# Kernel tuning notes

Measured on AMD Instinct MI355X. Metric: run time of the kernel, lower is better.

## Reference

```python
import jax, jax.numpy as jnp
import numpy as np

PRED_LEN = 12
A = 128          # agents in the single scene
NHEAD = 8
NLAYERS = 2
D = 256          # embedding_dim
MLP = 1024
HDIM = 128       # decoder_h_dim
OBS_LEN = 8
MEMLEN = A * OBS_LEN
NEG = -1e9       # stands in for float('-inf') in the AR mask


def _sinusoid(length, d):
    pos = jnp.arange(length, dtype=jnp.float32)[:, None]
    div = jnp.exp(jnp.arange(0, d, 2, dtype=jnp.float32) * (-np.log(10000.0) / d))
    ang = pos * div
    pe = jnp.zeros((length, d), jnp.float32)
    pe = pe.at[:, 0::2].set(jnp.sin(ang))
    pe = pe.at[:, 1::2].set(jnp.cos(ang))
    return pe


def _ln(x, g, b):
    m = x.mean(-1, keepdims=True)
    v = ((x - m) ** 2).mean(-1, keepdims=True)
    return (x - m) / jnp.sqrt(v + 1e-5) * g + b


def _mha(q, k, v, Wq, bq, Wk, bk, Wv, bv, Wo, bo, mask):
    dh = D // NHEAD
    qh = (q @ Wq.T + bq).reshape(-1, NHEAD, dh)
    kh = (k @ Wk.T + bk).reshape(-1, NHEAD, dh)
    vh = (v @ Wv.T + bv).reshape(-1, NHEAD, dh)
    s = jnp.einsum('ihd,jhd->hij', qh, kh) / np.sqrt(dh) + mask[None]
    w = jax.nn.softmax(s, axis=-1)
    o = jnp.einsum('hij,jhd->ihd', w, vh).reshape(-1, D)
    return o @ Wo.T + bo


def _forward(last_pos, decoder_state, memory, agent_mask, in_W, in_b, out_W, out_b,
             sa_Wq, sa_bq, sa_Wk, sa_bk, sa_Wv, sa_bv, sa_Wo, sa_bo,
             ca_Wq, ca_bq, ca_Wk, ca_bk, ca_Wv, ca_bv, ca_Wo, ca_bo,
             ff_W1, ff_b1, ff_W2, ff_b2,
             ln1_g, ln1_b, ln2_g, ln2_b, ln3_g, ln3_b):
    agent_pe = _sinusoid(A, D)
    scene_pos = last_pos
    tokens = []
    outs = []
    for s in range(PRED_LEN):  # fixed-length AR loop (unrolled, static shapes)
        feat = jnp.concatenate([scene_pos, decoder_state], axis=-1)  # [A, 2+HDIM]
        tokens.append(feat @ in_W.T + in_b)                          # [A, D]
        steps = s + 1
        tgt = jnp.concatenate(tokens, axis=0)                        # [steps*A, D]
        time_enc = jnp.repeat(_sinusoid(steps, D), A, axis=0)
        x = tgt + time_enc + jnp.tile(agent_pe, (steps, 1))
        times = jnp.repeat(jnp.arange(steps), A)
        # generate_ar_mask: block-causal over time, tiled agent_mask within block
        tgt_mask = jnp.where(times[None, :] > times[:, None], NEG,
                             jnp.tile(agent_mask, (steps, steps)))
        # generate_mask: tiled agent_mask for cross-attention to memory
        mem_mask = jnp.tile(agent_mask, (steps, MEMLEN // A))
        for l in range(NLAYERS):
            sa = _mha(x, x, x, sa_Wq[l], sa_bq[l], sa_Wk[l], sa_bk[l],
                      sa_Wv[l], sa_bv[l], sa_Wo[l], sa_bo[l], tgt_mask)
            x = _ln(x + sa, ln1_g[l], ln1_b[l])
            ca = _mha(x, memory, memory, ca_Wq[l], ca_bq[l], ca_Wk[l], ca_bk[l],
                      ca_Wv[l], ca_bv[l], ca_Wo[l], ca_bo[l], mem_mask)
            x = _ln(x + ca, ln2_g[l], ln2_b[l])
            ff = jax.nn.relu(x @ ff_W1[l].T + ff_b1[l]) @ ff_W2[l].T + ff_b2[l]
            x = _ln(x + ff, ln3_g[l], ln3_b[l])
        rel = x[-A:] @ out_W.T + out_b                               # [A, 2]
        outs.append(rel)
        scene_pos = scene_pos + rel
    return jnp.stack(outs, axis=0)                                   # [PRED_LEN, A, 2]


def setup_inputs():
    key = jax.random.key(0)
    ks = jax.random.split(key, 40)
    def rn(k, shape, scale=0.02):
        return jax.random.normal(k, shape, jnp.float32) * scale
    inp = {
        'last_pos': jax.random.normal(ks[0], (A, 2), jnp.float32),
        'decoder_state': jax.random.normal(ks[1], (A, HDIM), jnp.float32),
        'memory': jax.random.normal(ks[2], (MEMLEN, D), jnp.float32),
        'agent_mask': jnp.zeros((A, A), jnp.float32),
        'in_W': rn(ks[3], (D, 2 + HDIM)),
        'in_b': jnp.zeros((D,), jnp.float32),
        'out_W': rn(ks[4], (2, D)),
        'out_b': jnp.zeros((2,), jnp.float32),
    }
    names = ['sa_Wq', 'sa_Wk', 'sa_Wv', 'sa_Wo', 'ca_Wq', 'ca_Wk', 'ca_Wv', 'ca_Wo']
    for i, n in enumerate(names):
        inp[n] = rn(ks[5 + i], (NLAYERS, D, D))
        inp[n.replace('W', 'b')] = jnp.zeros((NLAYERS, D), jnp.float32)
    inp['ff_W1'] = rn(ks[20], (NLAYERS, MLP, D))
    inp['ff_b1'] = jnp.zeros((NLAYERS, MLP), jnp.float32)
    inp['ff_W2'] = rn(ks[21], (NLAYERS, D, MLP))
    inp['ff_b2'] = jnp.zeros((NLAYERS, D), jnp.float32)
    for n in ['ln1', 'ln2', 'ln3']:
        inp[n + '_g'] = jnp.ones((NLAYERS, D), jnp.float32)
        inp[n + '_b'] = jnp.zeros((NLAYERS, D), jnp.float32)
    return inp


def reference(last_pos, decoder_state, memory, agent_mask, in_W, in_b, out_W, out_b,
              sa_Wq, sa_bq, sa_Wk, sa_bk, sa_Wv, sa_bv, sa_Wo, sa_bo,
              ca_Wq, ca_bq, ca_Wk, ca_bk, ca_Wv, ca_bv, ca_Wo, ca_bo,
              ff_W1, ff_b1, ff_W2, ff_b2,
              ln1_g, ln1_b, ln2_g, ln2_b, ln3_g, ln3_b):
    return _forward(last_pos, decoder_state, memory, agent_mask, in_W, in_b, out_W, out_b,
                    sa_Wq, sa_bq, sa_Wk, sa_bk, sa_Wv, sa_bv, sa_Wo, sa_bo,
                    ca_Wq, ca_bq, ca_Wk, ca_bk, ca_Wv, ca_bv, ca_Wo, ca_bo,
                    ff_W1, ff_b1, ff_W2, ff_b2,
                    ln1_g, ln1_b, ln2_g, ln2_b, ln3_g, ln3_b)
```

## Files before the change

### kernel.cpp

```cpp
#include <hip/hip_runtime.h>
#include <math.h>

#define AGENTS 128
#define DIM 256
#define NHEADS 8
#define MEM_LEN 1024
#define MLP_DIM 1024
#define PRED 12
#define MAXS (PRED * AGENTS)

typedef __attribute__((ext_vector_type(8))) short short8;
typedef __attribute__((ext_vector_type(4))) float f32x4;

#define MFMA(a, b, c) __builtin_amdgcn_mfma_f32_16x16x32_bf16(a, b, c, 0, 0, 0)

__device__ __forceinline__ unsigned short f2bf(float f) {
  union { float f; unsigned u; } v; v.f = f;
  unsigned r = v.u + 0x7fffu + ((v.u >> 16) & 1u);
  return (unsigned short)(r >> 16);
}

__device__ __forceinline__ short8 afrag8(const float* p) {
  float4 a = *(const float4*)p;
  float4 b = *(const float4*)(p + 4);
  short8 r;
  r[0] = (short)f2bf(a.x); r[1] = (short)f2bf(a.y);
  r[2] = (short)f2bf(a.z); r[3] = (short)f2bf(a.w);
  r[4] = (short)f2bf(b.x); r[5] = (short)f2bf(b.y);
  r[6] = (short)f2bf(b.z); r[7] = (short)f2bf(b.w);
  return r;
}

__device__ __forceinline__ void ln_stats(const float* __restrict__ pst, int row,
                                         float& mean, float& rstd) {
  float4 p0 = *(const float4*)(pst + row * 8);
  float4 p1 = *(const float4*)(pst + row * 8 + 4);
  float s  = p0.x + p0.z + p1.x + p1.z;
  float ss = p0.y + p0.w + p1.y + p1.w;
  mean = s * (1.0f / 256.0f);
  rstd = rsqrtf(ss * (1.0f / 256.0f) - mean * mean + 1e-5f);
}

__device__ __forceinline__ short8 afragLN(const float* __restrict__ yr,
                                          const float* __restrict__ lg,
                                          const float* __restrict__ lb,
                                          int k, float mean, float rstd) {
  float4 a = *(const float4*)(yr + k), b = *(const float4*)(yr + k + 4);
  float4 ga = *(const float4*)(lg + k), gb = *(const float4*)(lg + k + 4);
  float4 ba = *(const float4*)(lb + k), bb = *(const float4*)(lb + k + 4);
  short8 r;
  r[0] = (short)f2bf((a.x - mean) * rstd * ga.x + ba.x);
  r[1] = (short)f2bf((a.y - mean) * rstd * ga.y + ba.y);
  r[2] = (short)f2bf((a.z - mean) * rstd * ga.z + ba.z);
  r[3] = (short)f2bf((a.w - mean) * rstd * ga.w + ba.w);
  r[4] = (short)f2bf((b.x - mean) * rstd * gb.x + bb.x);
  r[5] = (short)f2bf((b.y - mean) * rstd * gb.y + bb.y);
  r[6] = (short)f2bf((b.z - mean) * rstd * gb.z + bb.z);
  r[7] = (short)f2bf((b.w - mean) * rstd * gb.w + bb.w);
  return r;
}

template <int AMODE, int RES, int EPI>
__global__ __launch_bounds__(256) void wproj_k(
    const unsigned short* __restrict__ ab, int lda,
    const float* __restrict__ Ya, const float* __restrict__ psta,
    const float* __restrict__ lga, const float* __restrict__ lba,
    const unsigned short* __restrict__ W, const float* __restrict__ bias, int K,
    const float* __restrict__ res,
    const float* __restrict__ Yp, const float* __restrict__ pstp,
    const float* __restrict__ gp, const float* __restrict__ bp,
    float* __restrict__ Yo, float* __restrict__ psto,
    unsigned short* __restrict__ mido)
{
  const int tid = threadIdx.x, l = tid & 63, w = tid >> 6;
  const int c15 = l & 15, g8 = (l >> 4) * 8, r0v = (l >> 4) * 4;
  const int rowb = blockIdx.x * 64 + w * 16;
  const int arow = rowb + c15;
  const int cb = blockIdx.y;
  const int colb = cb * 64;

  float meanA = 0.f, rstdA = 0.f;
  if (AMODE == 1) ln_stats(psta, arow, meanA, rstdA);

  const int KC = K >> 5;
  f32x4 acc[4] = {};
  const unsigned short* wp = W + (colb + c15) * K + g8;
  for (int kc = 0; kc < KC; ++kc) {
    short8 af;
    if (AMODE == 0) af = *(const short8*)(ab + arow * lda + kc * 32 + g8);
    else af = afragLN(Ya + arow * 256, lga, lba, kc * 32 + g8, meanA, rstdA);
#pragma unroll
    for (int t = 0; t < 4; ++t)
      acc[t] = MFMA(af, *(const short8*)(wp + t * 16 * K + kc * 32), acc[t]);
  }

  float mp[4], rp[4];
  if (RES == 2) {
#pragma unroll
    for (int r = 0; r < 4; ++r) ln_stats(pstp, rowb + r0v + r, mp[r], rp[r]);
  }

  float v[4][4];
#pragma unroll
  for (int t = 0; t < 4; ++t) {
    const int col = colb + t * 16 + c15;
    const float bb = bias[col];
    float gpp = 0.f, bpp = 0.f;
    if (RES == 2) { gpp = gp[col]; bpp = bp[col]; }
#pragma unroll
    for (int r = 0; r < 4; ++r) {
      const int row = rowb + r0v + r;
      float x = acc[t][r] + bb;
      if (RES == 1) x += res[row * 256 + col];
      if (RES == 2) x += (Yp[row * 256 + col] - mp[r]) * rp[r] * gpp + bpp;
      if (EPI == 0) Yo[row * 256 + col] = x;
      if (EPI == 1) mido[row * 1024 + col] = f2bf(fmaxf(x, 0.f));
      v[t][r] = x;
    }
  }
  if (EPI == 0) {
#pragma unroll
    for (int r = 0; r < 4; ++r) {
      float s  = v[0][r] + v[1][r] + v[2][r] + v[3][r];
      float ss = v[0][r]*v[0][r] + v[1][r]*v[1][r] + v[2][r]*v[2][r] + v[3][r]*v[3][r];
#pragma unroll
      for (int m = 1; m < 16; m <<= 1) {
        s  += __shfl_xor(s, m, 64);
        ss += __shfl_xor(ss, m, 64);
      }
      if (c15 == 0) {
        const int row = rowb + r0v + r;
        psto[row * 8 + cb * 2]     = s;
        psto[row * 8 + cb * 2 + 1] = ss;
      }
    }
  }
}

template <int AMODE>
__global__ __launch_bounds__(256) void kvproj_k(
    const unsigned short* __restrict__ ab, int lda,
    const float* __restrict__ Ya, const float* __restrict__ psta,
    const float* __restrict__ lga, const float* __restrict__ lba,
    const float* __restrict__ af32,
    const unsigned short* __restrict__ Wk, const float* __restrict__ bk,
    const unsigned short* __restrict__ Wv, const float* __restrict__ bv,
    unsigned short* __restrict__ Ko, unsigned short* __restrict__ Vo,
    int Spad, int crow)
{
  const int tid = threadIdx.x, l = tid & 63, w = tid >> 6;
  const int c15 = l & 15, g8 = (l >> 4) * 8, r0v = (l >> 4) * 4;
  const int rowb = blockIdx.x * 64 + w * 16;
  const int arow = rowb + c15;
  const int y = blockIdx.y;
  const bool isK = y < 4;
  const int colb = (y & 3) * 64;
  const unsigned short* W = isK ? Wk : Wv;
  const float* bias = isK ? bk : bv;

  float meanA = 0.f, rstdA = 0.f;
  if (AMODE == 1) ln_stats(psta, arow, meanA, rstdA);

  f32x4 acc[4] = {};
  const unsigned short* wp = W + (colb + c15) * 256 + g8;
  for (int kc = 0; kc < 8; ++kc) {
    short8 af;
    if (AMODE == 0) af = *(const short8*)(ab + arow * lda + kc * 32 + g8);
    else if (AMODE == 1) af = afragLN(Ya + arow * 256, lga, lba, kc * 32 + g8, meanA, rstdA);
    else af = afrag8(af32 + arow * 256 + kc * 32 + g8);
#pragma unroll
    for (int t = 0; t < 4; ++t)
      acc[t] = MFMA(af, *(const short8*)(wp + t * 16 * 256 + kc * 32), acc[t]);
  }
#pragma unroll
  for (int t = 0; t < 4; ++t) {
    const int col = colb + t * 16 + c15;
    const float bb = bias[col];
    const int hh = col >> 5, d = col & 31;
#pragma unroll
    for (int r = 0; r < 4; ++r) {
      const int row = crow + rowb + r0v + r;
      unsigned short val = f2bf(acc[t][r] + bb);
      if (isK) Ko[hh * Spad * 32 + row * 32 + d] = val;
      else     Vo[col * Spad + row] = val;
    }
  }
}

template <int AMODE>
__global__ __launch_bounds__(256) void attn2_k(
    const unsigned short* __restrict__ ab,
    const float* __restrict__ Ya, const float* __restrict__ psta,
    const float* __restrict__ lga, const float* __restrict__ lba,
    const unsigned short* __restrict__ Wq, const float* __restrict__ bq,
    const unsigned short* __restrict__ Kc, const unsigned short* __restrict__ Vt,
    const float* __restrict__ mask, unsigned short* __restrict__ Ob,
    int S, int Spad)
{
  __shared__ unsigned short sq[4][16][32];
  __shared__ unsigned short ps[4][16][96];
  const int tid = threadIdx.x, l = tid & 63, w = tid >> 6;
  const int c15 = l & 15, g = l >> 4, g8 = g * 8, r0v = g * 4;
  const int h = blockIdx.y;
  const int rowb = blockIdx.x * 64 + w * 16;
  const int arow = rowb + c15;

  float meanA = 0.f, rstdA = 0.f;
  if (AMODE == 1) ln_stats(psta, arow, meanA, rstdA);
  f32x4 q0 = {}, q1 = {};
  const unsigned short* wp = Wq + (h * 32 + c15) * 256 + g8;
  for (int kc = 0; kc < 8; ++kc) {
    short8 af;
    if (AMODE == 0) af = *(const short8*)(ab + arow * 256 + kc * 32 + g8);
    else af = afragLN(Ya + arow * 256, lga, lba, kc * 32 + g8, meanA, rstdA);
    q0 = MFMA(af, *(const short8*)(wp + kc * 32), q0);
    q1 = MFMA(af, *(const short8*)(wp + 16 * 256 + kc * 32), q1);
  }
  {
    const float b0 = bq[h * 32 + c15], b1 = bq[h * 32 + 16 + c15];
#pragma unroll
    for (int r = 0; r < 4; ++r) {
      sq[w][r0v + r][c15]      = f2bf(q0[r] + b0);
      sq[w][r0v + r][16 + c15] = f2bf(q1[r] + b1);
    }
  }
  short8 qf = *(const short8*)&sq[w][c15][g8];

  float mk[2][4][4];
#pragma unroll
  for (int p = 0; p < 2; ++p)
#pragma unroll
    for (int t = 0; t < 4; ++t)
#pragma unroll
      for (int r = 0; r < 4; ++r)
        mk[p][t][r] = mask[arow * AGENTS + p * 64 + t * 16 + g * 4 + r];

  const unsigned short* kh = Kc + h * Spad * 32;
  const unsigned short* vh = Vt + h * 32 * Spad;
  unsigned short* pq = &ps[w][0][0];
  const float scale = 0.17677669529663687f;
  f32x4 oa0 = {}, oa1 = {};
  float lsum = 0.f;

  for (int kc = 0; kc < S; kc += 64) {
    const int p = (kc >> 6) & 1;
#pragma unroll
    for (int t = 0; t < 4; ++t) {
      short8 kf = *(const short8*)(kh + (kc + t * 16 + c15) * 32 + g8);
      f32x4 zz = {};
      f32x4 sc = MFMA(kf, qf, zz);
      float e0 = __expf(sc[0] * scale + mk[p][t][0]);
      float e1 = __expf(sc[1] * scale + mk[p][t][1]);
      float e2 = __expf(sc[2] * scale + mk[p][t][2]);
      float e3 = __expf(sc[3] * scale + mk[p][t][3]);
      unsigned short b0 = f2bf(e0), b1 = f2bf(e1), b2 = f2bf(e2), b3 = f2bf(e3);
      union { unsigned u; float f; } c0, c1, c2, c3;
      c0.u = (unsigned)b0 << 16; c1.u = (unsigned)b1 << 16;
      c2.u = (unsigned)b2 << 16; c3.u = (unsigned)b3 << 16;
      lsum += c0.f + c1.f + c2.f + c3.f;
      uint2 u2;
      u2.x = (unsigned)b0 | ((unsigned)b1 << 16);
      u2.y = (unsigned)b2 | ((unsigned)b3 << 16);
      *(uint2*)&pq[c15 * 96 + t * 16 + g * 4] = u2;
    }
#pragma unroll
    for (int ks = 0; ks < 2; ++ks) {
      short8 pf = *(const short8*)&pq[c15 * 96 + ks * 32 + g8];
      short8 v0 = *(const short8*)(vh + c15 * Spad + kc + ks * 32 + g8);
      short8 v1 = *(const short8*)(vh + (16 + c15) * Spad + kc + ks * 32 + g8);
      oa0 = MFMA(v0, pf, oa0);
      oa1 = MFMA(v1, pf, oa1);
    }
  }
  lsum += __shfl_xor(lsum, 16, 64);
  lsum += __shfl_xor(lsum, 32, 64);
  const float inv = 1.0f / lsum;
#pragma unroll
  for (int r = 0; r < 4; ++r) {
    Ob[arow * DIM + h * 32 + g * 4 + r]      = f2bf(oa0[r] * inv);
    Ob[arow * DIM + h * 32 + 16 + g * 4 + r] = f2bf(oa1[r] * inv);
  }
}

__global__ __launch_bounds__(256) void embed_k(
    const float* __restrict__ scene, const float* __restrict__ ds,
    const unsigned short* __restrict__ inWb, const float* __restrict__ inb,
    const float* __restrict__ peA, const float* __restrict__ peT,
    float* __restrict__ x0, unsigned short* __restrict__ xb0, int step)
{
  const int tid = threadIdx.x, l = tid & 63, w = tid >> 6;
  const int c15 = l & 15, g8 = (l >> 4) * 8, r0v = (l >> 4) * 4;
  const int rowb = blockIdx.x * 64 + w * 16;
  const int arow = rowb + c15;
  const int colb = blockIdx.y * 64;
  f32x4 acc[4] = {};
  const unsigned short* wp = inWb + (colb + c15) * 160 + g8;
  for (int kc = 0; kc < 5; ++kc) {
    short8 af;
#pragma unroll
    for (int j = 0; j < 8; ++j) {
      int kk = kc * 32 + g8 + j;
      float v = (kk < 2) ? scene[arow * 2 + kk]
                         : ((kk < 130) ? ds[arow * 128 + (kk - 2)] : 0.f);
      af[j] = (short)f2bf(v);
    }
#pragma unroll
    for (int t = 0; t < 4; ++t)
      acc[t] = MFMA(af, *(const short8*)(wp + t * 16 * 160 + kc * 32), acc[t]);
  }
#pragma unroll
  for (int t = 0; t < 4; ++t) {
    const int col = colb + t * 16 + c15;
    const float bb = inb[col] + peT[step * DIM + col];
#pragma unroll
    for (int r = 0; r < 4; ++r) {
      const int row = rowb + r0v + r;
      float v = acc[t][r] + bb + peA[row * DIM + col];
      x0[row * DIM + col] = v;
      xb0[row * DIM + col] = f2bf(v);
    }
  }
}

__global__ __launch_bounds__(256) void outp_k(
    const float* __restrict__ Y3, const float* __restrict__ pst3,
    const float* __restrict__ g3, const float* __restrict__ b3,
    const float* __restrict__ outW, const float* __restrict__ outB,
    float* __restrict__ outbuf, float* __restrict__ scene, int step)
{
  const int tid = threadIdx.x;
  const int row = tid >> 1, j = tid & 1;
  float mean, rstd;
  ln_stats(pst3, row, mean, rstd);
  const float* yr = Y3 + row * 256;
  const float* wr = outW + j * 256;
  float a = 0.f;
  for (int k = 0; k < 256; k += 4) {
    float4 y = *(const float4*)(yr + k);
    float4 gg = *(const float4*)(g3 + k);
    float4 bb = *(const float4*)(b3 + k);
    float4 ww = *(const float4*)(wr + k);
    a += ((y.x - mean) * rstd * gg.x + bb.x) * ww.x
       + ((y.y - mean) * rstd * gg.y + bb.y) * ww.y
       + ((y.z - mean) * rstd * gg.z + bb.z) * ww.z
       + ((y.w - mean) * rstd * gg.w + bb.w) * ww.w;
  }
  a += outB[j];
  outbuf[(step * AGENTS + row) * 2 + j] = a;
  scene[row * 2 + j] += a;
}

__global__ void cvt8_k(const float* p0, const float* p1, const float* p2,
                       const float* p3, const float* p4, const float* p5,
                       const float* p6, const float* p7, unsigned short* dst)
{
  const float* s;
  switch (blockIdx.z) {
    case 0: s = p0; break; case 1: s = p1; break;
    case 2: s = p2; break; case 3: s = p3; break;
    case 4: s = p4; break; case 5: s = p5; break;
    case 6: s = p6; break; default: s = p7; break;
  }
  int i = blockIdx.x * 256 + threadIdx.x;
  dst[blockIdx.z * 131072 + i] = f2bf(s[i]);
}

__global__ void cvtff_k(const float* w1, const float* w2, unsigned short* dst)
{
  const float* s = blockIdx.z ? w2 : w1;
  int i = blockIdx.x * 256 + threadIdx.x;
  dst[blockIdx.z * 524288 + i] = f2bf(s[i]);
}

__global__ void cvtinw_k(const float* w, unsigned short* dst)
{
  int i = blockIdx.x * 256 + threadIdx.x;
  if (i >= 256 * 160) return;
  int n = i / 160, k = i - n * 160;
  dst[i] = (k < 130) ? f2bf(w[n * 130 + k]) : (unsigned short)0;
}

__global__ void pe_k(float* peA, float* peT)
{
  int i = blockIdx.x * 256 + threadIdx.x;
  if (i < 128 * 256) {
    int row = i >> 8, c = i & 255, p = c >> 1;
    float dv = expf((float)(2 * p) * (-9.210340371976184f / 256.f));
    float ang = (float)row * dv;
    peA[i] = (c & 1) ? cosf(ang) : sinf(ang);
  } else if (i < 140 * 256) {
    int j = i - 32768;
    int s = j >> 8, c = j & 255, p = c >> 1;
    float dv = expf((float)(2 * p) * (-9.210340371976184f / 256.f));
    float ang = (float)s * dv;
    peT[j] = (c & 1) ? cosf(ang) : sinf(ang);
  }
}

extern "C" void kernel_launch(void* const* d_in, const int* in_sizes, int n_in,
                              void* d_out, int out_size, void* d_ws, size_t ws_size,
                              hipStream_t stream)
{
  const float* last_pos      = (const float*)d_in[0];
  const float* decoder_state = (const float*)d_in[1];
  const float* memory        = (const float*)d_in[2];
  const float* agent_mask    = (const float*)d_in[3];
  const float* in_W  = (const float*)d_in[4];
  const float* in_b  = (const float*)d_in[5];
  const float* out_W = (const float*)d_in[6];
  const float* out_b = (const float*)d_in[7];
  const float* sa_bq = (const float*)d_in[9];
  const float* sa_bk = (const float*)d_in[11];
  const float* sa_bv = (const float*)d_in[13];
  const float* sa_bo = (const float*)d_in[15];
  const float* ca_bq = (const float*)d_in[17];
  const float* ca_bk = (const float*)d_in[19];
  const float* ca_bv = (const float*)d_in[21];
  const float* ca_bo = (const float*)d_in[23];
  const float* ff_W1 = (const float*)d_in[24];
  const float* ff_b1 = (const float*)d_in[25];
  const float* ff_W2 = (const float*)d_in[26];
  const float* ff_b2 = (const float*)d_in[27];
  const float* ln1_g = (const float*)d_in[28];
  const float* ln1_b = (const float*)d_in[29];
  const float* ln2_g = (const float*)d_in[30];
  const float* ln2_b = (const float*)d_in[31];
  const float* ln3_g = (const float*)d_in[32];
  const float* ln3_b = (const float*)d_in[33];
  float* out = (float*)d_out;

  float* ws    = (float*)d_ws;
  float* scene = ws;
  float* x0    = scene + 256;
  float* Y1    = x0 + 32768;
  float* Y2    = Y1 + 32768;
  float* Y3    = Y2 + 32768;
  float* pst1  = Y3 + 32768;
  float* pst2  = pst1 + 1024;
  float* pst3  = pst2 + 1024;
  float* peA   = pst3 + 1024;
  float* peT   = peA + 32768;
  unsigned short* xb0   = (unsigned short*)(peT + 3072);
  unsigned short* abuf  = xb0 + 32768;
  unsigned short* mid   = abuf + 32768;
  unsigned short* saK   = mid + 131072;
  unsigned short* saV   = saK + 2 * MAXS * 256;
  unsigned short* memK  = saV + 2 * MAXS * 256;
  unsigned short* memV  = memK + 2 * MEM_LEN * 256;
  unsigned short* dxdb  = memV + 2 * MEM_LEN * 256;
  unsigned short* ffW1b = dxdb + 8 * 131072;
  unsigned short* ffW2b = ffW1b + 524288;
  unsigned short* inWb  = ffW2b + 524288;

  const dim3 blk(256);

  cvt8_k<<<dim3(512, 1, 8), blk, 0, stream>>>(
      (const float*)d_in[8], (const float*)d_in[10], (const float*)d_in[12],
      (const float*)d_in[14], (const float*)d_in[16], (const float*)d_in[18],
      (const float*)d_in[20], (const float*)d_in[22], dxdb);
  cvtff_k<<<dim3(2048, 1, 2), blk, 0, stream>>>(ff_W1, ff_W2, ffW1b);
  cvtinw_k<<<160, blk, 0, stream>>>(in_W, inWb);
  pe_k<<<140, blk, 0, stream>>>(peA, peT);
  for (int l = 0; l < 2; ++l) {
    kvproj_k<2><<<dim3(16, 8), blk, 0, stream>>>(
        nullptr, 0, nullptr, nullptr, nullptr, nullptr, memory,
        dxdb + 5 * 131072 + l * 65536, ca_bk + l * 256,
        dxdb + 6 * 131072 + l * 65536, ca_bv + l * 256,
        memK + l * 262144, memV + l * 262144, MEM_LEN, 0);
  }
  hipMemcpyAsync(scene, last_pos, 256 * sizeof(float), hipMemcpyDeviceToDevice, stream);

  for (int s = 0; s < PRED; ++s) {
    embed_k<<<dim3(2, 4), blk, 0, stream>>>(scene, decoder_state, inWb, in_b,
                                            peA, peT, x0, xb0, s);
    for (int l = 0; l < 2; ++l) {
      const unsigned short* saWq = dxdb + 0 * 131072 + l * 65536;
      const unsigned short* saWk = dxdb + 1 * 131072 + l * 65536;
      const unsigned short* saWv = dxdb + 2 * 131072 + l * 65536;
      const unsigned short* saWo = dxdb + 3 * 131072 + l * 65536;
      const unsigned short* caWq = dxdb + 4 * 131072 + l * 65536;
      const unsigned short* caWo = dxdb + 7 * 131072 + l * 65536;
      unsigned short* saKl = saK + l * MAXS * 256;
      unsigned short* saVl = saV + l * MAXS * 256;
      unsigned short* memKl = memK + l * 262144;
      unsigned short* memVl = memV + l * 262144;

      if (l == 0) {
        kvproj_k<0><<<dim3(2, 8), blk, 0, stream>>>(
            xb0, 256, nullptr, nullptr, nullptr, nullptr, nullptr,
            saWk, sa_bk, saWv, sa_bv, saKl, saVl, MAXS, s * AGENTS);
        attn2_k<0><<<dim3(2, 8), blk, 0, stream>>>(
            xb0, nullptr, nullptr, nullptr, nullptr,
            saWq, sa_bq, saKl, saVl, agent_mask, abuf, (s + 1) * AGENTS, MAXS);
        wproj_k<0, 1, 0><<<dim3(2, 4), blk, 0, stream>>>(
            abuf, 256, nullptr, nullptr, nullptr, nullptr,
            saWo, sa_bo, 256, x0, nullptr, nullptr, nullptr, nullptr,
            Y1, pst1, nullptr);
      } else {
        kvproj_k<1><<<dim3(2, 8), blk, 0, stream>>>(
            nullptr, 0, Y3, pst3, ln3_g, ln3_b, nullptr,
            saWk, sa_bk + 256, saWv, sa_bv + 256, saKl, saVl, MAXS, s * AGENTS);
        attn2_k<1><<<dim3(2, 8), blk, 0, stream>>>(
            nullptr, Y3, pst3, ln3_g, ln3_b,
            saWq, sa_bq + 256, saKl, saVl, agent_mask, abuf, (s + 1) * AGENTS, MAXS);
        wproj_k<0, 2, 0><<<dim3(2, 4), blk, 0, stream>>>(
            abuf, 256, nullptr, nullptr, nullptr, nullptr,
            saWo, sa_bo + 256, 256, nullptr, Y3, pst3, ln3_g, ln3_b,
            Y1, pst1, nullptr);
      }
      attn2_k<1><<<dim3(2, 8), blk, 0, stream>>>(
          nullptr, Y1, pst1, ln1_g + l * 256, ln1_b + l * 256,
          caWq, ca_bq + l * 256, memKl, memVl, agent_mask, abuf, MEM_LEN, MEM_LEN);
      wproj_k<0, 2, 0><<<dim3(2, 4), blk, 0, stream>>>(
          abuf, 256, nullptr, nullptr, nullptr, nullptr,
          caWo, ca_bo + l * 256, 256, nullptr, Y1, pst1, ln1_g + l * 256, ln1_b + l * 256,
          Y2, pst2, nullptr);
      wproj_k<1, 0, 1><<<dim3(2, 16), blk, 0, stream>>>(
          nullptr, 0, Y2, pst2, ln2_g + l * 256, ln2_b + l * 256,
          ffW1b + l * 262144, ff_b1 + l * 1024, 256,
          nullptr, nullptr, nullptr, nullptr, nullptr,
          nullptr, nullptr, mid);
      wproj_k<0, 2, 0><<<dim3(2, 4), blk, 0, stream>>>(
          mid, 1024, nullptr, nullptr, nullptr, nullptr,
          ffW2b + l * 262144, ff_b2 + l * 256, 1024,
          nullptr, Y2, pst2, ln2_g + l * 256, ln2_b + l * 256,
          Y3, pst3, nullptr);
    }
    outp_k<<<1, blk, 0, stream>>>(Y3, pst3, ln3_g + 256, ln3_b + 256,
                                  out_W, out_b, out, scene, s);
  }
}
```

Measured before the change: 2.481 ms.

## Fuse autoregressive decoder loop into persistent megakernel with grid barriers

Replaces roughly 170 small kernel launches for the 12-step AR decoder with one persistent 16-workgroup kernel that runs each stage as a phase and separates phases with a software grid barrier. The output projection is folded into the next step's embed phase, and the per-step scene positions are kept in an array so no in-place update races across workgroups. The memory K/V projections for both layers are merged into a single launch. This targets launch overhead and inter-kernel gaps. In exchange it adds atomic barrier cost, relies on all 16 workgroups being co-resident, and leaves most of the GPU idle within each phase.

```diff
diff --git a/kernel.cpp b/kernel.cpp
--- a/kernel.cpp
+++ b/kernel.cpp
@@ -5,9 +5,9 @@
 #define DIM 256
 #define NHEADS 8
 #define MEM_LEN 1024
-#define MLP_DIM 1024
 #define PRED 12
 #define MAXS (PRED * AGENTS)
+#define NWG 16
 
 typedef __attribute__((ext_vector_type(8))) short short8;
 typedef __attribute__((ext_vector_type(4))) float f32x4;
@@ -60,89 +60,113 @@
   return r;
 }
 
-template <int AMODE, int RES, int EPI>
-__global__ __launch_bounds__(256) void wproj_k(
-    const unsigned short* __restrict__ ab, int lda,
+struct MegaP {
+  const float *ds, *mask;
+  const float *in_b, *out_W, *out_b;
+  const float *sa_bq, *sa_bk, *sa_bv, *sa_bo;
+  const float *ca_bq, *ca_bo;
+  const float *ff_b1, *ff_b2;
+  const float *ln1_g, *ln1_b, *ln2_g, *ln2_b, *ln3_g, *ln3_b;
+  float *out;
+  float *sceneArr;
+  float *x0, *Y1, *Y2, *Y3;
+  float *pst1, *pst2, *pst3;
+  const float *peA, *peT;
+  unsigned short *xb0, *abuf, *mid;
+  unsigned short *saK, *saV, *memK, *memV;
+  const unsigned short *dxdb, *ffW1b, *ffW2b, *inWb;
+  unsigned *barCnt, *barGen;
+};
+
+__device__ __forceinline__ void gridbar(unsigned* cnt, unsigned* gen) {
+  __syncthreads();
+  if (threadIdx.x == 0) {
+    __threadfence();
+    unsigned g = __hip_atomic_load(gen, __ATOMIC_RELAXED, __HIP_MEMORY_SCOPE_AGENT);
+    unsigned a = __hip_atomic_fetch_add(cnt, 1u, __ATOMIC_ACQ_REL, __HIP_MEMORY_SCOPE_AGENT);
+    if (a == (unsigned)(NWG - 1)) {
+      __hip_atomic_store(cnt, 0u, __ATOMIC_RELAXED, __HIP_MEMORY_SCOPE_AGENT);
+      __hip_atomic_store(gen, g + 1u, __ATOMIC_RELEASE, __HIP_MEMORY_SCOPE_AGENT);
+    } else {
+      while (__hip_atomic_load(gen, __ATOMIC_ACQUIRE, __HIP_MEMORY_SCOPE_AGENT) == g)
+        __builtin_amdgcn_s_sleep(1);
+    }
+    __threadfence();
+  }
+  __syncthreads();
+}
+
+__device__ void embed_phase(const MegaP& p, int wg, int s) {
+  if (wg >= 8) return;
+  __shared__ float sscene[256];
+  const int tid = threadIdx.x;
+  if (s > 0) {
+    const int row = tid >> 1, j = tid & 1;
+    float mean, rstd; ln_stats(p.pst3, row, mean, rstd);
+    const float* yr = p.Y3 + row * 256;
+    const float* wr = p.out_W + j * 256;
+    const float* g3 = p.ln3_g + 256;
+    const float* b3 = p.ln3_b + 256;
+    float a = 0.f;
+    for (int k = 0; k < 256; k += 4) {
+      float4 y = *(const float4*)(yr + k);
+      float4 gg = *(const float4*)(g3 + k);
+      float4 bb = *(const float4*)(b3 + k);
+      float4 ww = *(const float4*)(wr + k);
+      a += ((y.x - mean) * rstd * gg.x + bb.x) * ww.x
+         + ((y.y - mean) * rstd * gg.y + bb.y) * ww.y
+         + ((y.z - mean) * rstd * gg.z + bb.z) * ww.z
+         + ((y.w - mean) * rstd * gg.w + bb.w) * ww.w;
+    }
+    a += p.out_b[j];
+    float sv = p.sceneArr[(s - 1) * 256 + row * 2 + j] + a;
+    if (wg == 0) p.out[((s - 1) * AGENTS + row) * 2 + j] = a;
+    p.sceneArr[s * 256 + row * 2 + j] = sv;
+    sscene[row * 2 + j] = sv;
+  } else {
+    sscene[tid] = p.sceneArr[tid];
+  }
+  __syncthreads();
+
+  const int l = tid & 63, w = tid >> 6;
+  const int c15 = l & 15, g8 = (l >> 4) * 8, r0v = (l >> 4) * 4;
+  const int rowb = (wg >> 2) * 64 + w * 16;
+  const int arow = rowb + c15;
+  const int colb = (wg & 3) * 64;
+  f32x4 acc[4] = {};
+  const unsigned short* wp = p.inWb + (colb + c15) * 160 + g8;
+  for (int kc = 0; kc < 5; ++kc) {
+    short8 af;
+#pragma unroll
+    for (int j = 0; j < 8; ++j) {
+      int kk = kc * 32 + g8 + j;
+      float v = (kk < 2) ? sscene[arow * 2 + kk]
+                         : ((kk < 130) ? p.ds[arow * 128 + (kk - 2)] : 0.f);
+      af[j] = (short)f2bf(v);
+    }
+#pragma unroll
+    for (int t = 0; t < 4; ++t)
+      acc[t] = MFMA(af, *(const short8*)(wp + t * 16 * 160 + kc * 32), acc[t]);
+  }
+#pragma unroll
+  for (int t = 0; t < 4; ++t) {
+    const int col = colb + t * 16 + c15;
+    const float bb = p.in_b[col] + p.peT[s * DIM + col];
+#pragma unroll
+    for (int r = 0; r < 4; ++r) {
+      const int row = rowb + r0v + r;
+      float v = acc[t][r] + bb + p.peA[row * DIM + col];
+      p.x0[row * DIM + col] = v;
+      p.xb0[row * DIM + col] = f2bf(v);
+    }
+  }
+}
+
+template <int AMODE>
+__device__ void kv_phase(const MegaP& p, int wg,
+    const unsigned short* __restrict__ ab,
     const float* __restrict__ Ya, const float* __restrict__ psta,
     const float* __restrict__ lga, const float* __restrict__ lba,
-    const unsigned short* __restrict__ W, const float* __restrict__ bias, int K,
-    const float* __restrict__ res,
-    const float* __restrict__ Yp, const float* __restrict__ pstp,
-    const float* __restrict__ gp, const float* __restrict__ bp,
-    float* __restrict__ Yo, float* __restrict__ psto,
-    unsigned short* __restrict__ mido)
-{
-  const int tid = threadIdx.x, l = tid & 63, w = tid >> 6;
-  const int c15 = l & 15, g8 = (l >> 4) * 8, r0v = (l >> 4) * 4;
-  const int rowb = blockIdx.x * 64 + w * 16;
-  const int arow = rowb + c15;
-  const int cb = blockIdx.y;
-  const int colb = cb * 64;
-
-  float meanA = 0.f, rstdA = 0.f;
-  if (AMODE == 1) ln_stats(psta, arow, meanA, rstdA);
-
-  const int KC = K >> 5;
-  f32x4 acc[4] = {};
-  const unsigned short* wp = W + (colb + c15) * K + g8;
-  for (int kc = 0; kc < KC; ++kc) {
-    short8 af;
-    if (AMODE == 0) af = *(const short8*)(ab + arow * lda + kc * 32 + g8);
-    else af = afragLN(Ya + arow * 256, lga, lba, kc * 32 + g8, meanA, rstdA);
-#pragma unroll
-    for (int t = 0; t < 4; ++t)
-      acc[t] = MFMA(af, *(const short8*)(wp + t * 16 * K + kc * 32), acc[t]);
-  }
-
-  float mp[4], rp[4];
-  if (RES == 2) {
-#pragma unroll
-    for (int r = 0; r < 4; ++r) ln_stats(pstp, rowb + r0v + r, mp[r], rp[r]);
-  }
-
-  float v[4][4];
-#pragma unroll
-  for (int t = 0; t < 4; ++t) {
-    const int col = colb + t * 16 + c15;
-    const float bb = bias[col];
-    float gpp = 0.f, bpp = 0.f;
-    if (RES == 2) { gpp = gp[col]; bpp = bp[col]; }
-#pragma unroll
-    for (int r = 0; r < 4; ++r) {
-      const int row = rowb + r0v + r;
-      float x = acc[t][r] + bb;
-      if (RES == 1) x += res[row * 256 + col];
-      if (RES == 2) x += (Yp[row * 256 + col] - mp[r]) * rp[r] * gpp + bpp;
-      if (EPI == 0) Yo[row * 256 + col] = x;
-      if (EPI == 1) mido[row * 1024 + col] = f2bf(fmaxf(x, 0.f));
-      v[t][r] = x;
-    }
-  }
-  if (EPI == 0) {
-#pragma unroll
-    for (int r = 0; r < 4; ++r) {
-      float s  = v[0][r] + v[1][r] + v[2][r] + v[3][r];
-      float ss = v[0][r]*v[0][r] + v[1][r]*v[1][r] + v[2][r]*v[2][r] + v[3][r]*v[3][r];
-#pragma unroll
-      for (int m = 1; m < 16; m <<= 1) {
-        s  += __shfl_xor(s, m, 64);
-        ss += __shfl_xor(ss, m, 64);
-      }
-      if (c15 == 0) {
-        const int row = rowb + r0v + r;
-        psto[row * 8 + cb * 2]     = s;
-        psto[row * 8 + cb * 2 + 1] = ss;
-      }
-    }
-  }
-}
-
-template <int AMODE>
-__global__ __launch_bounds__(256) void kvproj_k(
-    const unsigned short* __restrict__ ab, int lda,
-    const float* __restrict__ Ya, const float* __restrict__ psta,
-    const float* __restrict__ lga, const float* __restrict__ lba,
-    const float* __restrict__ af32,
     const unsigned short* __restrict__ Wk, const float* __restrict__ bk,
     const unsigned short* __restrict__ Wv, const float* __restrict__ bv,
     unsigned short* __restrict__ Ko, unsigned short* __restrict__ Vo,
@@ -150,9 +174,9 @@
 {
   const int tid = threadIdx.x, l = tid & 63, w = tid >> 6;
   const int c15 = l & 15, g8 = (l >> 4) * 8, r0v = (l >> 4) * 4;
-  const int rowb = blockIdx.x * 64 + w * 16;
+  const int rowb = (wg >> 3) * 64 + w * 16;
   const int arow = rowb + c15;
-  const int y = blockIdx.y;
+  const int y = wg & 7;
   const bool isK = y < 4;
   const int colb = (y & 3) * 64;
   const unsigned short* W = isK ? Wk : Wv;
@@ -165,9 +189,8 @@
   const unsigned short* wp = W + (colb + c15) * 256 + g8;
   for (int kc = 0; kc < 8; ++kc) {
     short8 af;
-    if (AMODE == 0) af = *(const short8*)(ab + arow * lda + kc * 32 + g8);
-    else if (AMODE == 1) af = afragLN(Ya + arow * 256, lga, lba, kc * 32 + g8, meanA, rstdA);
-    else af = afrag8(af32 + arow * 256 + kc * 32 + g8);
+    if (AMODE == 0) af = *(const short8*)(ab + arow * 256 + kc * 32 + g8);
+    else af = afragLN(Ya + arow * 256, lga, lba, kc * 32 + g8, meanA, rstdA);
 #pragma unroll
     for (int t = 0; t < 4; ++t)
       acc[t] = MFMA(af, *(const short8*)(wp + t * 16 * 256 + kc * 32), acc[t]);
@@ -188,21 +211,20 @@
 }
 
 template <int AMODE>
-__global__ __launch_bounds__(256) void attn2_k(
+__device__ void attn_phase(const MegaP& p, int wg,
     const unsigned short* __restrict__ ab,
     const float* __restrict__ Ya, const float* __restrict__ psta,
     const float* __restrict__ lga, const float* __restrict__ lba,
     const unsigned short* __restrict__ Wq, const float* __restrict__ bq,
     const unsigned short* __restrict__ Kc, const unsigned short* __restrict__ Vt,
-    const float* __restrict__ mask, unsigned short* __restrict__ Ob,
-    int S, int Spad)
+    unsigned short* __restrict__ Ob, int S, int Spad)
 {
   __shared__ unsigned short sq[4][16][32];
   __shared__ unsigned short ps[4][16][96];
   const int tid = threadIdx.x, l = tid & 63, w = tid >> 6;
   const int c15 = l & 15, g = l >> 4, g8 = g * 8, r0v = g * 4;
-  const int h = blockIdx.y;
-  const int rowb = blockIdx.x * 64 + w * 16;
+  const int h = wg & 7;
+  const int rowb = (wg >> 3) * 64 + w * 16;
   const int arow = rowb + c15;
 
   float meanA = 0.f, rstdA = 0.f;
@@ -228,12 +250,12 @@
 
   float mk[2][4][4];
 #pragma unroll
-  for (int p = 0; p < 2; ++p)
+  for (int pp = 0; pp < 2; ++pp)
 #pragma unroll
     for (int t = 0; t < 4; ++t)
 #pragma unroll
       for (int r = 0; r < 4; ++r)
-        mk[p][t][r] = mask[arow * AGENTS + p * 64 + t * 16 + g * 4 + r];
+        mk[pp][t][r] = p.mask[arow * AGENTS + pp * 64 + t * 16 + g * 4 + r];
 
   const unsigned short* kh = Kc + h * Spad * 32;
   const unsigned short* vh = Vt + h * 32 * Spad;
@@ -243,16 +265,16 @@
   float lsum = 0.f;
 
   for (int kc = 0; kc < S; kc += 64) {
-    const int p = (kc >> 6) & 1;
+    const int pp = (kc >> 6) & 1;
 #pragma unroll
     for (int t = 0; t < 4; ++t) {
       short8 kf = *(const short8*)(kh + (kc + t * 16 + c15) * 32 + g8);
       f32x4 zz = {};
       f32x4 sc = MFMA(kf, qf, zz);
-      float e0 = __expf(sc[0] * scale + mk[p][t][0]);
-      float e1 = __expf(sc[1] * scale + mk[p][t][1]);
-      float e2 = __expf(sc[2] * scale + mk[p][t][2]);
-      float e3 = __expf(sc[3] * scale + mk[p][t][3]);
+      float e0 = __expf(sc[0] * scale + mk[pp][t][0]);
+      float e1 = __expf(sc[1] * scale + mk[pp][t][1]);
+      float e2 = __expf(sc[2] * scale + mk[pp][t][2]);
+      float e3 = __expf(sc[3] * scale + mk[pp][t][3]);
       unsigned short b0 = f2bf(e0), b1 = f2bf(e1), b2 = f2bf(e2), b3 = f2bf(e3);
       union { unsigned u; float f; } c0, c1, c2, c3;
       c0.u = (unsigned)b0 << 16; c1.u = (unsigned)b1 << 16;
@@ -282,58 +304,110 @@
   }
 }
 
-__global__ __launch_bounds__(256) void embed_k(
-    const float* __restrict__ scene, const float* __restrict__ ds,
-    const unsigned short* __restrict__ inWb, const float* __restrict__ inb,
-    const float* __restrict__ peA, const float* __restrict__ peT,
-    float* __restrict__ x0, unsigned short* __restrict__ xb0, int step)
-{
+template <int RES>
+__device__ void wproj_phase(const MegaP& p, int wg,
+    const unsigned short* __restrict__ ab, int lda,
+    const unsigned short* __restrict__ W, const float* __restrict__ bias, int K,
+    const float* __restrict__ res,
+    const float* __restrict__ Yp, const float* __restrict__ pstp,
+    const float* __restrict__ gp, const float* __restrict__ bp,
+    float* __restrict__ Yo, float* __restrict__ psto)
+{
+  if (wg >= 8) return;
   const int tid = threadIdx.x, l = tid & 63, w = tid >> 6;
   const int c15 = l & 15, g8 = (l >> 4) * 8, r0v = (l >> 4) * 4;
-  const int rowb = blockIdx.x * 64 + w * 16;
+  const int rowb = (wg >> 2) * 64 + w * 16;
   const int arow = rowb + c15;
-  const int colb = blockIdx.y * 64;
+  const int cb = wg & 3;
+  const int colb = cb * 64;
+
+  const int KC = K >> 5;
   f32x4 acc[4] = {};
-  const unsigned short* wp = inWb + (colb + c15) * 160 + g8;
-  for (int kc = 0; kc < 5; ++kc) {
-    short8 af;
-#pragma unroll
-    for (int j = 0; j < 8; ++j) {
-      int kk = kc * 32 + g8 + j;
-      float v = (kk < 2) ? scene[arow * 2 + kk]
-                         : ((kk < 130) ? ds[arow * 128 + (kk - 2)] : 0.f);
-      af[j] = (short)f2bf(v);
-    }
+  const unsigned short* wp = W + (colb + c15) * K + g8;
+  for (int kc = 0; kc < KC; ++kc) {
+    short8 af = *(const short8*)(ab + arow * lda + kc * 32 + g8);
 #pragma unroll
     for (int t = 0; t < 4; ++t)
-      acc[t] = MFMA(af, *(const short8*)(wp + t * 16 * 160 + kc * 32), acc[t]);
-  }
+      acc[t] = MFMA(af, *(const short8*)(wp + t * 16 * K + kc * 32), acc[t]);
+  }
+
+  float mp[4], rp[4];
+  if (RES == 2) {
+#pragma unroll
+    for (int r = 0; r < 4; ++r) ln_stats(pstp, rowb + r0v + r, mp[r], rp[r]);
+  }
+  float v[4][4];
 #pragma unroll
   for (int t = 0; t < 4; ++t) {
     const int col = colb + t * 16 + c15;
-    const float bb = inb[col] + peT[step * DIM + col];
+    const float bb = bias[col];
+    float gpp = 0.f, bpp = 0.f;
+    if (RES == 2) { gpp = gp[col]; bpp = bp[col]; }
 #pragma unroll
     for (int r = 0; r < 4; ++r) {
       const int row = rowb + r0v + r;
-      float v = acc[t][r] + bb + peA[row * DIM + col];
-      x0[row * DIM + col] = v;
-      xb0[row * DIM + col] = f2bf(v);
-    }
-  }
-}
-
-__global__ __launch_bounds__(256) void outp_k(
-    const float* __restrict__ Y3, const float* __restrict__ pst3,
-    const float* __restrict__ g3, const float* __restrict__ b3,
-    const float* __restrict__ outW, const float* __restrict__ outB,
-    float* __restrict__ outbuf, float* __restrict__ scene, int step)
-{
+      float x = acc[t][r] + bb;
+      if (RES == 1) x += res[row * 256 + col];
+      if (RES == 2) x += (Yp[row * 256 + col] - mp[r]) * rp[r] * gpp + bpp;
+      Yo[row * 256 + col] = x;
+      v[t][r] = x;
+    }
+  }
+#pragma unroll
+  for (int r = 0; r < 4; ++r) {
+    float s  = v[0][r] + v[1][r] + v[2][r] + v[3][r];
+    float ss = v[0][r]*v[0][r] + v[1][r]*v[1][r] + v[2][r]*v[2][r] + v[3][r]*v[3][r];
+#pragma unroll
+    for (int m = 1; m < 16; m <<= 1) {
+      s  += __shfl_xor(s, m, 64);
+      ss += __shfl_xor(ss, m, 64);
+    }
+    if (c15 == 0) {
+      const int row = rowb + r0v + r;
+      psto[row * 8 + cb * 2]     = s;
+      psto[row * 8 + cb * 2 + 1] = ss;
+    }
+  }
+}
+
+__device__ void ff1_phase(const MegaP& p, int wg,
+    const float* __restrict__ Ya, const float* __restrict__ psta,
+    const float* __restrict__ lga, const float* __restrict__ lba,
+    const unsigned short* __restrict__ W1, const float* __restrict__ b1)
+{
+  const int tid = threadIdx.x, l = tid & 63, w = tid >> 6;
+  const int c15 = l & 15, g8 = (l >> 4) * 8, r0v = (l >> 4) * 4;
+  const int rowb = (wg >> 3) * 64 + w * 16;
+  const int arow = rowb + c15;
+  const int colb = (wg & 7) * 128;
+  float mean, rstd; ln_stats(psta, arow, mean, rstd);
+  f32x4 acc[8] = {};
+  const unsigned short* wp = W1 + (colb + c15) * 256 + g8;
+  for (int kc = 0; kc < 8; ++kc) {
+    short8 af = afragLN(Ya + arow * 256, lga, lba, kc * 32 + g8, mean, rstd);
+#pragma unroll
+    for (int t = 0; t < 8; ++t)
+      acc[t] = MFMA(af, *(const short8*)(wp + t * 16 * 256 + kc * 32), acc[t]);
+  }
+#pragma unroll
+  for (int t = 0; t < 8; ++t) {
+    const int col = colb + t * 16 + c15;
+    const float bb = b1[col];
+#pragma unroll
+    for (int r = 0; r < 4; ++r)
+      p.mid[(rowb + r0v + r) * 1024 + col] = f2bf(fmaxf(acc[t][r] + bb, 0.f));
+  }
+}
+
+__device__ void final_phase(const MegaP& p, int wg) {
+  if (wg != 0) return;
   const int tid = threadIdx.x;
   const int row = tid >> 1, j = tid & 1;
-  float mean, rstd;
-  ln_stats(pst3, row, mean, rstd);
-  const float* yr = Y3 + row * 256;
-  const float* wr = outW + j * 256;
+  float mean, rstd; ln_stats(p.pst3, row, mean, rstd);
+  const float* yr = p.Y3 + row * 256;
+  const float* wr = p.out_W + j * 256;
+  const float* g3 = p.ln3_g + 256;
+  const float* b3 = p.ln3_b + 256;
   float a = 0.f;
   for (int k = 0; k < 256; k += 4) {
     float4 y = *(const float4*)(yr + k);
@@ -345,9 +419,68 @@
        + ((y.z - mean) * rstd * gg.z + bb.z) * ww.z
        + ((y.w - mean) * rstd * gg.w + bb.w) * ww.w;
   }
-  a += outB[j];
-  outbuf[(step * AGENTS + row) * 2 + j] = a;
-  scene[row * 2 + j] += a;
+  a += p.out_b[j];
+  p.out[((PRED - 1) * AGENTS + row) * 2 + j] = a;
+}
+
+__global__ __launch_bounds__(256, 1) void mega_k(MegaP p) {
+  const int wg = blockIdx.x;
+#define GB gridbar(p.barCnt, p.barGen)
+  for (int s = 0; s < PRED; ++s) {
+    embed_phase(p, wg, s);
+    GB;
+    for (int l = 0; l < 2; ++l) {
+      const unsigned short* saWq = p.dxdb + 0 * 131072 + l * 65536;
+      const unsigned short* saWk = p.dxdb + 1 * 131072 + l * 65536;
+      const unsigned short* saWv = p.dxdb + 2 * 131072 + l * 65536;
+      const unsigned short* saWo = p.dxdb + 3 * 131072 + l * 65536;
+      const unsigned short* caWq = p.dxdb + 4 * 131072 + l * 65536;
+      const unsigned short* caWo = p.dxdb + 7 * 131072 + l * 65536;
+      unsigned short* saKl = p.saK + l * MAXS * 256;
+      unsigned short* saVl = p.saV + l * MAXS * 256;
+      unsigned short* memKl = p.memK + l * 262144;
+      unsigned short* memVl = p.memV + l * 262144;
+
+      if (l == 0) {
+        kv_phase<0>(p, wg, p.xb0, nullptr, nullptr, nullptr, nullptr,
+                    saWk, p.sa_bk, saWv, p.sa_bv, saKl, saVl, MAXS, s * AGENTS);
+        GB;
+        attn_phase<0>(p, wg, p.xb0, nullptr, nullptr, nullptr, nullptr,
+                      saWq, p.sa_bq, saKl, saVl, p.abuf, (s + 1) * AGENTS, MAXS);
+        GB;
+        wproj_phase<1>(p, wg, p.abuf, 256, saWo, p.sa_bo, 256,
+                       p.x0, nullptr, nullptr, nullptr, nullptr, p.Y1, p.pst1);
+        GB;
+      } else {
+        kv_phase<1>(p, wg, nullptr, p.Y3, p.pst3, p.ln3_g, p.ln3_b,
+                    saWk, p.sa_bk + 256, saWv, p.sa_bv + 256, saKl, saVl,
+                    MAXS, s * AGENTS);
+        GB;
+        attn_phase<1>(p, wg, nullptr, p.Y3, p.pst3, p.ln3_g, p.ln3_b,
+                      saWq, p.sa_bq + 256, saKl, saVl, p.abuf, (s + 1) * AGENTS, MAXS);
+        GB;
+        wproj_phase<2>(p, wg, p.abuf, 256, saWo, p.sa_bo + 256, 256,
+                       nullptr, p.Y3, p.pst3, p.ln3_g, p.ln3_b, p.Y1, p.pst1);
+        GB;
+      }
+      attn_phase<1>(p, wg, nullptr, p.Y1, p.pst1, p.ln1_g + l * 256, p.ln1_b + l * 256,
+                    caWq, p.ca_bq + l * 256, memKl, memVl, p.abuf, MEM_LEN, MEM_LEN);
+      GB;
+      wproj_phase<2>(p, wg, p.abuf, 256, caWo, p.ca_bo + l * 256, 256,
+                     nullptr, p.Y1, p.pst1, p.ln1_g + l * 256, p.ln1_b + l * 256,
+                     p.Y2, p.pst2);
+      GB;
+      ff1_phase(p, wg, p.Y2, p.pst2, p.ln2_g + l * 256, p.ln2_b + l * 256,
+                p.ffW1b + l * 262144, p.ff_b1 + l * 1024);
+      GB;
+      wproj_phase<2>(p, wg, p.mid, 1024, p.ffW2b + l * 262144, p.ff_b2 + l * 256, 1024,
+                     nullptr, p.Y2, p.pst2, p.ln2_g + l * 256, p.ln2_b + l * 256,
+                     p.Y3, p.pst3);
+      GB;
+    }
+  }
+  final_phase(p, wg);
+#undef GB
 }
 
 __global__ void cvt8_k(const float* p0, const float* p1, const float* p2,
@@ -384,18 +517,60 @@
 {
   int i = blockIdx.x * 256 + threadIdx.x;
   if (i < 128 * 256) {
-    int row = i >> 8, c = i & 255, p = c >> 1;
-    float dv = expf((float)(2 * p) * (-9.210340371976184f / 256.f));
+    int row = i >> 8, c = i & 255, pp = c >> 1;
+    float dv = expf((float)(2 * pp) * (-9.210340371976184f / 256.f));
     float ang = (float)row * dv;
     peA[i] = (c & 1) ? cosf(ang) : sinf(ang);
   } else if (i < 140 * 256) {
     int j = i - 32768;
-    int s = j >> 8, c = j & 255, p = c >> 1;
-    float dv = expf((float)(2 * p) * (-9.210340371976184f / 256.f));
+    int s = j >> 8, c = j & 255, pp = c >> 1;
+    float dv = expf((float)(2 * pp) * (-9.210340371976184f / 256.f));
     float ang = (float)s * dv;
     peT[j] = (c & 1) ? cosf(ang) : sinf(ang);
   }
 }
+
+__global__ __launch_bounds__(256) void memkv_k(
+    const float* __restrict__ mem, const unsigned short* __restrict__ dxd,
+    const float* __restrict__ bk, const float* __restrict__ bvv,
+    unsigned short* __restrict__ memK, unsigned short* __restrict__ memV)
+{
+  const int li = blockIdx.z;
+  const int y = blockIdx.y;
+  const bool isK = y < 4;
+  const int colb = (y & 3) * 64;
+  const unsigned short* W = dxd + (isK ? 5 : 6) * 131072 + li * 65536;
+  const float* bias = (isK ? bk : bvv) + li * 256;
+  unsigned short* Ko = memK + li * MEM_LEN * 256;
+  unsigned short* Vo = memV + li * MEM_LEN * 256;
+  const int tid = threadIdx.x, l = tid & 63, w = tid >> 6;
+  const int c15 = l & 15, g8 = (l >> 4) * 8, r0v = (l >> 4) * 4;
+  const int rowb = blockIdx.x * 64 + w * 16;
+  const int arow = rowb + c15;
+  f32x4 acc[4] = {};
+  const unsigned short* wp = W + (colb + c15) * 256 + g8;
+  for (int kc = 0; kc < 8; ++kc) {
+    short8 af = afrag8(mem + arow * 256 + kc * 32 + g8);
+#pragma unroll
+    for (int t = 0; t < 4; ++t)
+      acc[t] = MFMA(af, *(const short8*)(wp + t * 16 * 256 + kc * 32), acc[t]);
+  }
+#pragma unroll
+  for (int t = 0; t < 4; ++t) {
+    const int col = colb + t * 16 + c15;
+    const float bb = bias[col];
+    const int hh = col >> 5, d = col & 31;
+#pragma unroll
+    for (int r = 0; r < 4; ++r) {
+      const int row = rowb + r0v + r;
+      unsigned short val = f2bf(acc[t][r] + bb);
+      if (isK) Ko[hh * MEM_LEN * 32 + row * 32 + d] = val;
+      else     Vo[col * MEM_LEN + row] = val;
+    }
+  }
+}
+
+__global__ void initbar_k(unsigned* b) { b[0] = 0; b[1] = 0; }
 
 extern "C" void kernel_launch(void* const* d_in, const int* in_sizes, int n_in,
                               void* d_out, int out_size, void* d_ws, size_t ws_size,
@@ -409,29 +584,10 @@
   const float* in_b  = (const float*)d_in[5];
   const float* out_W = (const float*)d_in[6];
   const float* out_b = (const float*)d_in[7];
-  const float* sa_bq = (const float*)d_in[9];
-  const float* sa_bk = (const float*)d_in[11];
-  const float* sa_bv = (const float*)d_in[13];
-  const float* sa_bo = (const float*)d_in[15];
-  const float* ca_bq = (const float*)d_in[17];
-  const float* ca_bk = (const float*)d_in[19];
-  const float* ca_bv = (const float*)d_in[21];
-  const float* ca_bo = (const float*)d_in[23];
-  const float* ff_W1 = (const float*)d_in[24];
-  const float* ff_b1 = (const float*)d_in[25];
-  const float* ff_W2 = (const float*)d_in[26];
-  const float* ff_b2 = (const float*)d_in[27];
-  const float* ln1_g = (const float*)d_in[28];
-  const float* ln1_b = (const float*)d_in[29];
-  const float* ln2_g = (const float*)d_in[30];
-  const float* ln2_b = (const float*)d_in[31];
-  const float* ln3_g = (const float*)d_in[32];
-  const float* ln3_b = (const float*)d_in[33];
-  float* out = (float*)d_out;
 
   float* ws    = (float*)d_ws;
-  float* scene = ws;
-  float* x0    = scene + 256;
+  float* sceneArr = ws;
+  float* x0    = sceneArr + 13 * 256;
   float* Y1    = x0 + 32768;
   float* Y2    = Y1 + 32768;
   float* Y3    = Y2 + 32768;
@@ -451,6 +607,7 @@
   unsigned short* ffW1b = dxdb + 8 * 131072;
   unsigned short* ffW2b = ffW1b + 524288;
   unsigned short* inWb  = ffW2b + 524288;
+  unsigned* bar = (unsigned*)(inWb + 40960);
 
   const dim3 blk(256);
 
@@ -458,75 +615,34 @@
       (const float*)d_in[8], (const float*)d_in[10], (const float*)d_in[12],
       (const float*)d_in[14], (const float*)d_in[16], (const float*)d_in[18],
       (const float*)d_in[20], (const float*)d_in[22], dxdb);
-  cvtff_k<<<dim3(2048, 1, 2), blk, 0, stream>>>(ff_W1, ff_W2, ffW1b);
+  cvtff_k<<<dim3(2048, 1, 2), blk, 0, stream>>>((const float*)d_in[24],
+                                                (const float*)d_in[26], ffW1b);
   cvtinw_k<<<160, blk, 0, stream>>>(in_W, inWb);
   pe_k<<<140, blk, 0, stream>>>(peA, peT);
-  for (int l = 0; l < 2; ++l) {
-    kvproj_k<2><<<dim3(16, 8), blk, 0, stream>>>(
-        nullptr, 0, nullptr, nullptr, nullptr, nullptr, memory,
-        dxdb + 5 * 131072 + l * 65536, ca_bk + l * 256,
-        dxdb + 6 * 131072 + l * 65536, ca_bv + l * 256,
-        memK + l * 262144, memV + l * 262144, MEM_LEN, 0);
-  }
-  hipMemcpyAsync(scene, last_pos, 256 * sizeof(float), hipMemcpyDeviceToDevice, stream);
-
-  for (int s = 0; s < PRED; ++s) {
-    embed_k<<<dim3(2, 4), blk, 0, stream>>>(scene, decoder_state, inWb, in_b,
-                                            peA, peT, x0, xb0, s);
-    for (int l = 0; l < 2; ++l) {
-      const unsigned short* saWq = dxdb + 0 * 131072 + l * 65536;
-      const unsigned short* saWk = dxdb + 1 * 131072 + l * 65536;
-      const unsigned short* saWv = dxdb + 2 * 131072 + l * 65536;
-      const unsigned short* saWo = dxdb + 3 * 131072 + l * 65536;
-      const unsigned short* caWq = dxdb + 4 * 131072 + l * 65536;
-      const unsigned short* caWo = dxdb + 7 * 131072 + l * 65536;
-      unsigned short* saKl = saK + l * MAXS * 256;
-      unsigned short* saVl = saV + l * MAXS * 256;
-      unsigned short* memKl = memK + l * 262144;
-      unsigned short* memVl = memV + l * 262144;
-
-      if (l == 0) {
-        kvproj_k<0><<<dim3(2, 8), blk, 0, stream>>>(
-            xb0, 256, nullptr, nullptr, nullptr, nullptr, nullptr,
-            saWk, sa_bk, saWv, sa_bv, saKl, saVl, MAXS, s * AGENTS);
-        attn2_k<0><<<dim3(2, 8), blk, 0, stream>>>(
-            xb0, nullptr, nullptr, nullptr, nullptr,
-            saWq, sa_bq, saKl, saVl, agent_mask, abuf, (s + 1) * AGENTS, MAXS);
-        wproj_k<0, 1, 0><<<dim3(2, 4), blk, 0, stream>>>(
-            abuf, 256, nullptr, nullptr, nullptr, nullptr,
-            saWo, sa_bo, 256, x0, nullptr, nullptr, nullptr, nullptr,
-            Y1, pst1, nullptr);
-      } else {
-        kvproj_k<1><<<dim3(2, 8), blk, 0, stream>>>(
-            nullptr, 0, Y3, pst3, ln3_g, ln3_b, nullptr,
-            saWk, sa_bk + 256, saWv, sa_bv + 256, saKl, saVl, MAXS, s * AGENTS);
-        attn2_k<1><<<dim3(2, 8), blk, 0, stream>>>(
-            nullptr, Y3, pst3, ln3_g, ln3_b,
-            saWq, sa_bq + 256, saKl, saVl, agent_mask, abuf, (s + 1) * AGENTS, MAXS);
-        wproj_k<0, 2, 0><<<dim3(2, 4), blk, 0, stream>>>(
-            abuf, 256, nullptr, nullptr, nullptr, nullptr,
-            saWo, sa_bo + 256, 256, nullptr, Y3, pst3, ln3_g, ln3_b,
-            Y1, pst1, nullptr);
-      }
-      attn2_k<1><<<dim3(2, 8), blk, 0, stream>>>(
-          nullptr, Y1, pst1, ln1_g + l * 256, ln1_b + l * 256,
-          caWq, ca_bq + l * 256, memKl, memVl, agent_mask, abuf, MEM_LEN, MEM_LEN);
-      wproj_k<0, 2, 0><<<dim3(2, 4), blk, 0, stream>>>(
-          abuf, 256, nullptr, nullptr, nullptr, nullptr,
-          caWo, ca_bo + l * 256, 256, nullptr, Y1, pst1, ln1_g + l * 256, ln1_b + l * 256,
-          Y2, pst2, nullptr);
-      wproj_k<1, 0, 1><<<dim3(2, 16), blk, 0, stream>>>(
-          nullptr, 0, Y2, pst2, ln2_g + l * 256, ln2_b + l * 256,
-          ffW1b + l * 262144, ff_b1 + l * 1024, 256,
-          nullptr, nullptr, nullptr, nullptr, nullptr,
-          nullptr, nullptr, mid);
-      wproj_k<0, 2, 0><<<dim3(2, 4), blk, 0, stream>>>(
-          mid, 1024, nullptr, nullptr, nullptr, nullptr,
-          ffW2b + l * 262144, ff_b2 + l * 256, 1024,
-          nullptr, Y2, pst2, ln2_g + l * 256, ln2_b + l * 256,
-          Y3, pst3, nullptr);
-    }
-    outp_k<<<1, blk, 0, stream>>>(Y3, pst3, ln3_g + 256, ln3_b + 256,
-                                  out_W, out_b, out, scene, s);
-  }
-}
+  memkv_k<<<dim3(16, 8, 2), blk, 0, stream>>>(memory, dxdb,
+      (const float*)d_in[19], (const float*)d_in[21], memK, memV);
+  initbar_k<<<1, 1, 0, stream>>>(bar);
+  hipMemcpyAsync(sceneArr, last_pos, 256 * sizeof(float),
+                 hipMemcpyDeviceToDevice, stream);
+
+  MegaP p;
+  p.ds = decoder_state; p.mask = agent_mask;
+  p.in_b = in_b; p.out_W = out_W; p.out_b = out_b;
+  p.sa_bq = (const float*)d_in[9];  p.sa_bk = (const float*)d_in[11];
+  p.sa_bv = (const float*)d_in[13]; p.sa_bo = (const float*)d_in[15];
+  p.ca_bq = (const float*)d_in[17]; p.ca_bo = (const float*)d_in[23];
+  p.ff_b1 = (const float*)d_in[25]; p.ff_b2 = (const float*)d_in[27];
+  p.ln1_g = (const float*)d_in[28]; p.ln1_b = (const float*)d_in[29];
+  p.ln2_g = (const float*)d_in[30]; p.ln2_b = (const float*)d_in[31];
+  p.ln3_g = (const float*)d_in[32]; p.ln3_b = (const float*)d_in[33];
+  p.out = (float*)d_out;
+  p.sceneArr = sceneArr; p.x0 = x0; p.Y1 = Y1; p.Y2 = Y2; p.Y3 = Y3;
+  p.pst1 = pst1; p.pst2 = pst2; p.pst3 = pst3;
+  p.peA = peA; p.peT = peT;
+  p.xb0 = xb0; p.abuf = abuf; p.mid = mid;
+  p.saK = saK; p.saV = saV; p.memK = memK; p.memV = memV;
+  p.dxdb = dxdb; p.ffW1b = ffW1b; p.ffW2b = ffW2b; p.inWb = inWb;
+  p.barCnt = bar; p.barGen = bar + 1;
+
+  mega_k<<<dim3(NWG), blk, 0, stream>>>(p);
+}
```

Result: slower. 3.690 ms (+48.7%).
